# Optimization experiments

Measured on AMD Instinct MI355X. Metric: run time of the kernel, lower is better.

## Reference

```python
import jax, jax.numpy as jnp
import numpy as np
import math

GRID = 256       # grid_size
KMAX = 64        # max_elements_per_cell
RES = 512        # image resolution
SPAN = 4         # max grid cells per axis covered by one triangle bbox
NUM_VIEWS = 16
SCALE = 0.5


def _projection_matrix(x=0.5, n=1.5, f=100.0):
    return np.array([[n / x, 0.0, 0.0, 0.0],
                     [0.0, n / -x, 0.0, 0.0],
                     [0.0, 0.0, -(f + n) / (f - n), -(2.0 * f * n) / (f - n)],
                     [0.0, 0.0, -1.0, 0.0]], dtype=np.float32)


def _view_buffers(num_views, seed):
    rng = np.random.default_rng(seed)
    proj = _projection_matrix()
    mvps, lights = [], []
    for _ in range(num_views):
        u1, u2, u3 = rng.random(3)
        qx = math.sqrt(1.0 - u1) * math.sin(math.tau * u2)
        qy = math.sqrt(1.0 - u1) * math.cos(math.tau * u2)
        qz = math.sqrt(u1) * math.sin(math.tau * u3)
        qw = math.sqrt(u1) * math.cos(math.tau * u3)
        rot = np.array([[1 - 2 * (qy * qy + qz * qz), 2 * (qx * qy - qz * qw), 2 * (qx * qz + qy * qw)],
                        [2 * (qx * qy + qz * qw), 1 - 2 * (qx * qx + qz * qz), 2 * (qy * qz - qx * qw)],
                        [2 * (qx * qz - qy * qw), 2 * (qy * qz + qx * qw), 1 - 2 * (qx * qx + qy * qy)]], dtype=np.float32)
        rmat = np.eye(4, dtype=np.float32); rmat[:3, :3] = rot
        tmat = np.eye(4, dtype=np.float32); tmat[2, 3] = -4.0
        view = tmat @ rmat
        campos = np.linalg.inv(view)[:3, 3]
        light = -campos / (np.linalg.norm(campos) + 1e-8)
        mvps.append(proj @ view)
        lights.append(light.astype(np.float32))
    return np.stack(mvps).astype(np.float32), np.stack(lights).astype(np.float32)


def setup_inputs() -> dict:
    key = jax.random.key(0)
    k1, k2 = jax.random.split(key)
    F = 100_000
    # clustered per-triangle vertices -> small on-screen triangles (mesh-like locality)
    centers = jax.random.uniform(k1, (F, 1, 3), minval=-1.0, maxval=1.0)
    jitter = jax.random.normal(k2, (F, 3, 3)) * 0.02
    u = (centers + jitter).reshape(-1, 3).astype(jnp.float32)          # [3F,3]
    faces = jnp.arange(3 * F, dtype=jnp.int32).reshape(F, 3)
    mvps, light = _view_buffers(NUM_VIEWS, 42)
    return {"u": u,
            "mvps": jnp.asarray(mvps),
            "lightdir": jnp.asarray(light),
            "background_color": jnp.zeros(3, jnp.float32),
            "base_colors": jnp.ones((F, 3), jnp.float32),
            "faces": faces}


def _forward(u, mvps, lightdir, background_color, base_colors, faces):
    # _normalize_vertices
    v = u - u.mean(0, keepdims=True)
    span = jnp.maximum(v.max() - v.min(), 1e-6)
    v = v * (SCALE / span)
    Fn = faces.shape[0]
    # project with active view 0 (v_hom @ mvps[0].T, no perspective divide, as in source)
    v_hom = jnp.concatenate([v, jnp.ones((v.shape[0], 1), v.dtype)], axis=1)
    v_ndc = v_hom @ mvps[0].T                                          # [V,4]
    tris = v_ndc[faces]                                                # [F,3,4]
    wtri = v[faces]                                                    # [F,3,3]
    nrm = jnp.cross(wtri[:, 0] - wtri[:, 1], wtri[:, 2] - wtri[:, 1])
    nrm = nrm / (jnp.linalg.norm(nrm, axis=-1, keepdims=True) + 1e-10)
    z = tris[:, :, 2].mean(1)
    order = jnp.argsort(z)                                             # depth sort (near first)
    st = tris[order]
    sn = nrm[order]
    cp = (st[:, :, :2] + 1.0) * 0.5                                    # [F,3,2] control pts in [0,1]
    shading = jnp.clip(jnp.sum(-lightdir[0] * sn, axis=-1, keepdims=True), 0.0)
    colors = base_colors[order] * shading                              # [F,3]
    # --- grid acceleration structure build (scatter triangles into cells) ---
    lo = jnp.clip(jnp.floor(cp.min(1) * GRID).astype(jnp.int32), 0, GRID - 1)  # [F,2]
    hi = jnp.clip(jnp.floor(cp.max(1) * GRID).astype(jnp.int32), 0, GRID - 1)
    d = jnp.arange(SPAN, dtype=jnp.int32)
    cx = lo[:, 0:1] + d[None, :]                                       # [F,SPAN]
    cy = lo[:, 1:2] + d[None, :]
    valid = (cy[:, :, None] <= hi[:, 1:2, None]) & (cx[:, None, :] <= hi[:, 0:1].reshape(Fn, 1, 1) + 0 * cx[:, None, :])
    valid = (cy[:, :, None] <= hi[:, 1:2, None]) & (cx[:, None, :] <= hi[:, 0:1][:, :, None])
    cell = cy[:, :, None] * GRID + cx[:, None, :]                      # [F,SPAN,SPAN]
    NC = GRID * GRID
    cell = jnp.where(valid, cell, NC).reshape(-1)
    tri = jnp.broadcast_to(jnp.arange(Fn, dtype=jnp.int32)[:, None, None], (Fn, SPAN, SPAN)).reshape(-1)
    # sort (cell, depth-rank): tri ids are already depth-ordered
    keys = cell.astype(jnp.int64) * (Fn + 1) + tri
    ordk = jnp.argsort(keys)
    sc = cell[ordk]
    stri = tri[ordk]
    counts = jax.ops.segment_sum(jnp.ones_like(sc), sc, num_segments=NC + 1)
    starts = jnp.concatenate([jnp.zeros(1, counts.dtype), jnp.cumsum(counts)[:-1]])
    rank = jnp.arange(sc.shape[0], dtype=jnp.int32) - starts[sc].astype(jnp.int32)
    ok = (rank < KMAX) & (sc < NC)
    grid_elems = jnp.full((NC + 1, KMAX), -1, jnp.int32)
    grid_elems = grid_elems.at[jnp.where(ok, sc, NC), jnp.where(ok, rank, 0)].set(jnp.where(ok, stri, -1))
    # --- per-pixel rasterization via grid query ---
    px = (jnp.arange(RES, dtype=jnp.float32) + 0.5) / RES
    uu, vv = jnp.meshgrid(px, px, indexing='xy')
    P = jnp.stack([uu, vv], -1).reshape(-1, 2)                         # [P,2]
    ix = jnp.clip((P[:, 0] * GRID).astype(jnp.int32), 0, GRID - 1)
    iy = jnp.clip((P[:, 1] * GRID).astype(jnp.int32), 0, GRID - 1)
    elems = grid_elems[iy * GRID + ix]                                 # [P,K]
    e = jnp.maximum(elems, 0)
    tpts = cp[e]                                                       # [P,K,3,2]
    a, b, c = tpts[:, :, 0], tpts[:, :, 1], tpts[:, :, 2]
    pp = P[:, None, :]

    def cr(o, q, r):
        return (q[..., 0] - o[..., 0]) * (r[..., 1] - o[..., 1]) - (q[..., 1] - o[..., 1]) * (r[..., 0] - o[..., 0])

    e0 = cr(a, b, pp)
    e1 = cr(b, c, pp)
    e2 = cr(c, a, pp)
    inside = ((e0 >= 0) & (e1 >= 0) & (e2 >= 0)) | ((e0 <= 0) & (e1 <= 0) & (e2 <= 0))
    hit = inside & (elems >= 0)
    first = jnp.argmax(hit, axis=1)                                    # front-most (depth-sorted)
    anyhit = jnp.any(hit, axis=1)
    tid = e[jnp.arange(e.shape[0]), first]
    img = jnp.where(anyhit[:, None], colors[tid], background_color[None, :])
    return img.reshape(RES, RES, 3)


def reference(u, mvps, lightdir, background_color, base_colors, faces):
    return _forward(u, mvps, lightdir, background_color, base_colors, faces)
```

## Files before the change

kernel.cpp:

```cpp
#include <hip/hip_runtime.h>
#include <stdint.h>

#pragma clang fp contract(off)

#define GRIDN 256
#define NC (GRIDN * GRIDN)
#define RESN 512
#define RBLOCKS 256
#define CAP 1024
#define CPB 16
#define NB 64
#define NS 16
#define SBINS 2048

typedef unsigned short bfraw;
typedef unsigned short u16;

__device__ __forceinline__ float bf2f(bfraw h) {
    return __uint_as_float(((uint32_t)h) << 16);
}
__device__ __forceinline__ bfraw f2bf(float f) {
    uint32_t b = __float_as_uint(f);
    return (bfraw)((b + 0x7FFFu + ((b >> 16) & 1u)) >> 16);
}
__device__ __forceinline__ uint32_t fkey(float f) {
    uint32_t b = __float_as_uint(f);
    return (b & 0x80000000u) ? ~b : (b | 0x80000000u);
}

__global__ __launch_bounds__(256) void k_reduce1(const bfraw* __restrict__ u, int nrows,
                                                 double* __restrict__ psum,
                                                 float* __restrict__ pmin,
                                                 float* __restrict__ pmax) {
    __shared__ double ssum[256 * 3];
    __shared__ float smin[256 * 3];
    __shared__ float smax[256 * 3];
    int t = threadIdx.x;
    double s0 = 0.0, s1 = 0.0, s2 = 0.0;
    float mn0 = INFINITY, mn1 = INFINITY, mn2 = INFINITY;
    float mx0 = -INFINITY, mx1 = -INFINITY, mx2 = -INFINITY;
    for (int r = blockIdx.x * 256 + t; r < nrows; r += 256 * RBLOCKS) {
        float a = bf2f(u[3 * r + 0]);
        float b = bf2f(u[3 * r + 1]);
        float c = bf2f(u[3 * r + 2]);
        s0 += (double)a; s1 += (double)b; s2 += (double)c;
        mn0 = fminf(mn0, a); mx0 = fmaxf(mx0, a);
        mn1 = fminf(mn1, b); mx1 = fmaxf(mx1, b);
        mn2 = fminf(mn2, c); mx2 = fmaxf(mx2, c);
    }
    ssum[t * 3 + 0] = s0; ssum[t * 3 + 1] = s1; ssum[t * 3 + 2] = s2;
    smin[t * 3 + 0] = mn0; smin[t * 3 + 1] = mn1; smin[t * 3 + 2] = mn2;
    smax[t * 3 + 0] = mx0; smax[t * 3 + 1] = mx1; smax[t * 3 + 2] = mx2;
    __syncthreads();
    for (int st = 128; st > 0; st >>= 1) {
        if (t < st) {
            for (int c = 0; c < 3; c++) {
                ssum[t * 3 + c] += ssum[(t + st) * 3 + c];
                smin[t * 3 + c] = fminf(smin[t * 3 + c], smin[(t + st) * 3 + c]);
                smax[t * 3 + c] = fmaxf(smax[t * 3 + c], smax[(t + st) * 3 + c]);
            }
        }
        __syncthreads();
    }
    if (t == 0) {
        for (int c = 0; c < 3; c++) {
            psum[blockIdx.x * 3 + c] = ssum[c];
            pmin[blockIdx.x * 3 + c] = smin[c];
            pmax[blockIdx.x * 3 + c] = smax[c];
        }
    }
}

__global__ __launch_bounds__(256) void k_reduce2(const double* __restrict__ psum,
                                                 const float* __restrict__ pmin,
                                                 const float* __restrict__ pmax,
                                                 int nrows, float* __restrict__ cst) {
    __shared__ double ssum[256 * 3];
    __shared__ float smin[256 * 3];
    __shared__ float smax[256 * 3];
    int t = threadIdx.x;
    for (int c = 0; c < 3; c++) {
        ssum[t * 3 + c] = psum[t * 3 + c];
        smin[t * 3 + c] = pmin[t * 3 + c];
        smax[t * 3 + c] = pmax[t * 3 + c];
    }
    __syncthreads();
    for (int st = 128; st > 0; st >>= 1) {
        if (t < st) {
            for (int c = 0; c < 3; c++) {
                ssum[t * 3 + c] += ssum[(t + st) * 3 + c];
                smin[t * 3 + c] = fminf(smin[t * 3 + c], smin[(t + st) * 3 + c]);
                smax[t * 3 + c] = fmaxf(smax[t * 3 + c], smax[(t + st) * 3 + c]);
            }
        }
        __syncthreads();
    }
    if (t == 0) {
        float fn = (float)nrows;
        float m0 = (float)ssum[0] / fn;
        float m1 = (float)ssum[1] / fn;
        float m2 = (float)ssum[2] / fn;
        float vmax = fmaxf(fmaxf(smax[0] - m0, smax[1] - m1), smax[2] - m2);
        float vmin = fminf(fminf(smin[0] - m0, smin[1] - m1), smin[2] - m2);
        float span = fmaxf(vmax - vmin, 1e-06f);
        float s = 0.5f / span;
        cst[0] = m0; cst[1] = m1; cst[2] = m2; cst[3] = s;
    }
}

__global__ __launch_bounds__(256) void k_setup(const bfraw* __restrict__ u,
                                               const int* __restrict__ faces,
                                               const bfraw* __restrict__ mvp,
                                               const bfraw* __restrict__ light,
                                               const float* __restrict__ cst,
                                               int F,
                                               float* __restrict__ tcs,
                                               uint32_t* __restrict__ tz,
                                               uint32_t* __restrict__ tbox) {
    int f = blockIdx.x * 256 + threadIdx.x;
    if (f >= F) return;
    float m0 = cst[0], m1 = cst[1], m2 = cst[2], s = cst[3];
    float M[12];
    for (int i = 0; i < 12; i++) M[i] = bf2f(mvp[i]);

    float vx[3], vy[3], vz[3], cpx[3], cpy[3], zc[3];
    for (int j = 0; j < 3; j++) {
        int idx = faces[3 * f + j];
        float a = bf2f(u[3 * idx + 0]);
        float b = bf2f(u[3 * idx + 1]);
        float c = bf2f(u[3 * idx + 2]);
        float x = (a - m0) * s;
        float y = (b - m1) * s;
        float z = (c - m2) * s;
        vx[j] = x; vy[j] = y; vz[j] = z;
        float cx = fmaf(x, M[0], 0.0f);
        cx = fmaf(y, M[1], cx); cx = fmaf(z, M[2], cx); cx = cx + M[3];
        float cy = fmaf(x, M[4], 0.0f);
        cy = fmaf(y, M[5], cy); cy = fmaf(z, M[6], cy); cy = cy + M[7];
        float cz = fmaf(x, M[8], 0.0f);
        cz = fmaf(y, M[9], cz); cz = fmaf(z, M[10], cz); cz = cz + M[11];
        cpx[j] = (cx + 1.0f) * 0.5f;
        cpy[j] = (cy + 1.0f) * 0.5f;
        zc[j] = cz;
    }
    float zmean = ((zc[0] + zc[1]) + zc[2]) / 3.0f;

    float e1x = vx[0] - vx[1], e1y = vy[0] - vy[1], e1z = vz[0] - vz[1];
    float e2x = vx[2] - vx[1], e2y = vy[2] - vy[1], e2z = vz[2] - vz[1];
    float nx = e1y * e2z - e1z * e2y;
    float ny = e1z * e2x - e1x * e2z;
    float nz = e1x * e2y - e1y * e2x;
    float nn = nx * nx;
    nn = nn + ny * ny;
    nn = nn + nz * nz;
    float d = sqrtf(nn) + 1e-10f;
    float inx = nx / d, iny = ny / d, inz = nz / d;

    float l0 = bf2f(light[0]), l1 = bf2f(light[1]), l2 = bf2f(light[2]);
    float p0 = (-l0) * inx;
    float p1 = (-l1) * iny;
    float p2 = (-l2) * inz;
    float shading = fmaxf((p0 + p1) + p2, 0.0f);

    tcs[f * 8 + 0] = cpx[0]; tcs[f * 8 + 1] = cpy[0];
    tcs[f * 8 + 2] = cpx[1]; tcs[f * 8 + 3] = cpy[1];
    tcs[f * 8 + 4] = cpx[2]; tcs[f * 8 + 5] = cpy[2];
    tcs[f * 8 + 6] = shading;
    tcs[f * 8 + 7] = 0.0f;

    tz[f] = fkey(zmean);

    float mnx = fminf(fminf(cpx[0], cpx[1]), cpx[2]);
    float mny = fminf(fminf(cpy[0], cpy[1]), cpy[2]);
    float mxx = fmaxf(fmaxf(cpx[0], cpx[1]), cpx[2]);
    float mxy = fmaxf(fmaxf(cpy[0], cpy[1]), cpy[2]);
    int lox = (int)floorf(mnx * 256.0f); lox = lox < 0 ? 0 : (lox > 255 ? 255 : lox);
    int loy = (int)floorf(mny * 256.0f); loy = loy < 0 ? 0 : (loy > 255 ? 255 : loy);
    int hix = (int)floorf(mxx * 256.0f); hix = hix < 0 ? 0 : (hix > 255 ? 255 : hix);
    int hiy = (int)floorf(mxy * 256.0f); hiy = hiy < 0 ? 0 : (hiy > 255 ? 255 : hiy);
    int hx = hix < lox + 3 ? hix : lox + 3;
    int hy = hiy < loy + 3 ? hiy : loy + 3;
    tbox[f] = (uint32_t)lox | ((uint32_t)loy << 8) | ((uint32_t)hx << 16) | ((uint32_t)hy << 24);
}

__global__ __launch_bounds__(256) void k_count(const uint32_t* __restrict__ tbox,
                                               int F,
                                               u16* __restrict__ blockHist) {
    __shared__ uint32_t hist[SBINS];
    int b = blockIdx.x >> 4;
    int sl = blockIdx.x & (NS - 1);
    int chunk = (F + NB - 1) / NB;
    int fs = b * chunk;
    int fe = fs + chunk < F ? fs + chunk : F;
    int y0 = sl * 16, y1 = y0 + 15;
    for (int i = threadIdx.x; i < SBINS; i += 256) hist[i] = 0u;
    __syncthreads();
    for (int f = fs + threadIdx.x; f < fe; f += 256) {
        uint32_t bx = tbox[f];
        int lox = bx & 255, loy = (bx >> 8) & 255;
        int hx = (bx >> 16) & 255, hy = bx >> 24;
        int ys = loy > y0 ? loy : y0;
        int ye = hy < y1 ? hy : y1;
        for (int yy = ys; yy <= ye; yy++) {
            for (int xx = lox; xx <= hx; xx++) {
                uint32_t c = (uint32_t)(yy * GRIDN + xx) & 4095u;
                atomicAdd(&hist[c >> 1], 1u << (16u * (c & 1u)));
            }
        }
    }
    __syncthreads();
    uint32_t* dst = (uint32_t*)(blockHist + (size_t)b * NC) + sl * SBINS;
    for (int i = threadIdx.x; i < SBINS; i += 256) dst[i] = hist[i];
}

__global__ __launch_bounds__(1024) void k_scanA1(u16* __restrict__ blockHist,
                                                 uint32_t* __restrict__ cellOff,
                                                 uint32_t* __restrict__ blockSum) {
    __shared__ uint32_t sc[1024];
    int B = blockIdx.x, t = threadIdx.x;
    int c = B * 1024 + t;
    uint32_t tot = 0;
    for (int b = 0; b < NB; b++) {
        size_t o = (size_t)b * NC + c;
        uint32_t v = blockHist[o];
        blockHist[o] = (u16)tot;
        tot += v;
    }
    sc[t] = tot;
    __syncthreads();
    for (int st = 1; st < 1024; st <<= 1) {
        uint32_t a = 0;
        if (t >= st) a = sc[t - st];
        __syncthreads();
        if (t >= st) sc[t] += a;
        __syncthreads();
    }
    cellOff[c] = sc[t] - tot;
    if (t == 1023) blockSum[B] = sc[1023];
}

__global__ __launch_bounds__(1024) void k_scanB(uint32_t* __restrict__ cellOff,
                                                const uint32_t* __restrict__ blockSum) {
    __shared__ uint32_t pre[65];
    int B = blockIdx.x, t = threadIdx.x;
    if (t == 0) {
        uint32_t run = 0;
        for (int i = 0; i < 64; i++) { pre[i] = run; run += blockSum[i]; }
        pre[64] = run;
    }
    __syncthreads();
    cellOff[B * 1024 + t] += pre[B];
    if (B == 63 && t == 1023) cellOff[NC] = pre[64];
}

__global__ __launch_bounds__(256) void k_place(const uint32_t* __restrict__ tbox,
                                               const u16* __restrict__ blockHist,
                                               const uint32_t* __restrict__ cellOff,
                                               uint32_t* __restrict__ pairs,
                                               int F) {
    __shared__ uint32_t hist[SBINS];
    int b = blockIdx.x >> 4;
    int sl = blockIdx.x & (NS - 1);
    int chunk = (F + NB - 1) / NB;
    int fs = b * chunk;
    int fe = fs + chunk < F ? fs + chunk : F;
    int y0 = sl * 16, y1 = y0 + 15;
    uint32_t pcap = (uint32_t)F * 16u;
    for (int i = threadIdx.x; i < SBINS; i += 256) hist[i] = 0u;
    __syncthreads();
    for (int f = fs + threadIdx.x; f < fe; f += 256) {
        uint32_t bx = tbox[f];
        int lox = bx & 255, loy = (bx >> 8) & 255;
        int hx = (bx >> 16) & 255, hy = bx >> 24;
        int ys = loy > y0 ? loy : y0;
        int ye = hy < y1 ? hy : y1;
        for (int yy = ys; yy <= ye; yy++) {
            for (int xx = lox; xx <= hx; xx++) {
                uint32_t cell = (uint32_t)(yy * GRIDN + xx);
                uint32_t c = cell & 4095u;
                uint32_t sh = 16u * (c & 1u);
                uint32_t old = atomicAdd(&hist[c >> 1], 1u << sh);
                uint32_t r = (old >> sh) & 0xFFFFu;
                uint32_t pos = cellOff[cell] + (uint32_t)blockHist[(size_t)b * NC + cell] + r;
                if (pos < pcap) pairs[pos] = (uint32_t)f;
            }
        }
    }
}

__global__ __launch_bounds__(256) void k_cellsort(const uint32_t* __restrict__ cellOff,
                                                  const uint32_t* __restrict__ tz,
                                                  uint32_t* __restrict__ pairs,
                                                  int F) {
    __shared__ uint64_t lkeys[CAP];
    uint32_t pcap = (uint32_t)F * 16u;
    int t = threadIdx.x;
    int cell0 = blockIdx.x * CPB;
    for (int ci = 0; ci < CPB; ci++) {
        int cell = cell0 + ci;
        uint32_t off = cellOff[cell];
        uint32_t end = cellOff[cell + 1];
        if (off > pcap || end > pcap || end < off) continue;
        uint32_t n = end - off;
        if (n <= 64u) continue;
        uint32_t m = n > CAP ? CAP : n;
        for (uint32_t i = t; i < m; i += 256) {
            uint32_t id = pairs[off + i];
            if (id >= (uint32_t)F) id = 0;
            lkeys[i] = ((uint64_t)tz[id] << 32) | id;
        }
        __syncthreads();
        uint64_t k0 = ~0ull, k1 = ~0ull, k2 = ~0ull, k3 = ~0ull;
        uint32_t i0 = t, i1 = t + 256, i2 = t + 512, i3 = t + 768;
        if (i0 < m) k0 = lkeys[i0];
        if (i1 < m) k1 = lkeys[i1];
        if (i2 < m) k2 = lkeys[i2];
        if (i3 < m) k3 = lkeys[i3];
        uint32_t r0 = 0, r1 = 0, r2 = 0, r3 = 0;
        for (uint32_t j = 0; j < m; j++) {
            uint64_t kj = lkeys[j];
            r0 += (kj < k0) ? 1u : 0u;
            r1 += (kj < k1) ? 1u : 0u;
            r2 += (kj < k2) ? 1u : 0u;
            r3 += (kj < k3) ? 1u : 0u;
        }
        if (i0 < m && r0 < 64u) pairs[off + r0] = (uint32_t)(k0 & 0xFFFFFFFFu);
        if (i1 < m && r1 < 64u) pairs[off + r1] = (uint32_t)(k1 & 0xFFFFFFFFu);
        if (i2 < m && r2 < 64u) pairs[off + r2] = (uint32_t)(k2 & 0xFFFFFFFFu);
        if (i3 < m && r3 < 64u) pairs[off + r3] = (uint32_t)(k3 & 0xFFFFFFFFu);
        __syncthreads();
    }
}

__global__ __launch_bounds__(256) void k_raster(const float* __restrict__ tcs,
                                                const uint32_t* __restrict__ tz,
                                                const uint32_t* __restrict__ cellOff,
                                                const uint32_t* __restrict__ pairs,
                                                const bfraw* __restrict__ basec,
                                                const bfraw* __restrict__ bg,
                                                bfraw* __restrict__ out, int F) {
    int p = blockIdx.x * 256 + threadIdx.x;
    int col = p & (RESN - 1);
    int row = p >> 9;
    float px = ((float)col + 0.5f) / 512.0f;
    float py = ((float)row + 0.5f) / 512.0f;
    int cell = (row >> 1) * GRIDN + (col >> 1);
    uint32_t pcap = (uint32_t)F * 16u;
    uint32_t off = cellOff[cell];
    uint32_t end = cellOff[cell + 1];
    uint32_t m = 0;
    if (off <= pcap && end <= pcap && end >= off) {
        uint32_t n = end - off;
        m = n > 64u ? 64u : n;
    }
    uint64_t best = ~0ull;
    float bestSh = 0.0f;
    for (uint32_t k = 0; k < m; k++) {
        uint32_t id = pairs[off + k];
        if (id >= (uint32_t)F) continue;
        const float4 A = *(const float4*)(tcs + (size_t)id * 8);
        const float4 B = *(const float4*)(tcs + (size_t)id * 8 + 4);
        float ax = A.x, ay = A.y, bx = A.z, by = A.w, cx = B.x, cy = B.y;
        float e0 = (bx - ax) * (py - ay) - (by - ay) * (px - ax);
        float e1 = (cx - bx) * (py - by) - (cy - by) * (px - bx);
        float e2 = (ax - cx) * (py - cy) - (ay - cy) * (px - cx);
        bool inside = (e0 >= 0.0f && e1 >= 0.0f && e2 >= 0.0f) ||
                      (e0 <= 0.0f && e1 <= 0.0f && e2 <= 0.0f);
        if (inside) {
            uint64_t key = ((uint64_t)tz[id] << 32) | id;
            if (key < best) { best = key; bestSh = B.z; }
        }
    }
    float r, g, b;
    if (best != ~0ull) {
        uint32_t id = (uint32_t)(best & 0xFFFFFFFFu);
        r = bf2f(basec[3 * id + 0]) * bestSh;
        g = bf2f(basec[3 * id + 1]) * bestSh;
        b = bf2f(basec[3 * id + 2]) * bestSh;
    } else {
        r = bf2f(bg[0]); g = bf2f(bg[1]); b = bf2f(bg[2]);
    }
    int o = p * 3;
    out[o + 0] = f2bf(r);
    out[o + 1] = f2bf(g);
    out[o + 2] = f2bf(b);
}

__global__ __launch_bounds__(256) void k_diag(bfraw* __restrict__ out, float code) {
    out[blockIdx.x * 256 + threadIdx.x] = f2bf(code);
}

extern "C" void kernel_launch(void* const* d_in, const int* in_sizes, int n_in,
                              void* d_out, int out_size, void* d_ws, size_t ws_size,
                              hipStream_t stream) {
    const bfraw* u = (const bfraw*)d_in[0];
    const bfraw* mvps = (const bfraw*)d_in[1];
    const bfraw* light = (const bfraw*)d_in[2];
    const bfraw* bg = (const bfraw*)d_in[3];
    const bfraw* basec = (const bfraw*)d_in[4];
    const int* faces = (const int*)d_in[5];
    int nrows = in_sizes[0] / 3;
    int F = in_sizes[5] / 3;
    bfraw* out = (bfraw*)d_out;

    char* w = (char*)d_ws;
    size_t off = 0;
    auto alloc = [&](size_t bytes) -> void* {
        off = (off + 255) & ~(size_t)255;
        void* p = w + off;
        off += bytes;
        return p;
    };

    float* cst = (float*)alloc(4 * sizeof(float));
    double* psum = (double*)alloc((size_t)RBLOCKS * 3 * sizeof(double));
    float* pmin = (float*)alloc((size_t)RBLOCKS * 3 * sizeof(float));
    float* pmax = (float*)alloc((size_t)RBLOCKS * 3 * sizeof(float));
    float* tcs = (float*)alloc((size_t)F * 8 * sizeof(float));
    uint32_t* tz = (uint32_t*)alloc((size_t)F * sizeof(uint32_t));
    uint32_t* tbox = (uint32_t*)alloc((size_t)F * sizeof(uint32_t));
    u16* blockHist = (u16*)alloc((size_t)NB * NC * sizeof(u16));
    uint32_t* cellOff = (uint32_t*)alloc(((size_t)NC + 1) * sizeof(uint32_t));
    uint32_t* blockSum = (uint32_t*)alloc(64 * sizeof(uint32_t));
    uint32_t* pairs = (uint32_t*)alloc((size_t)F * 16 * sizeof(uint32_t));
    size_t needed = off;

    if (ws_size < needed) {
        float code = 20000.0f + (float)(ws_size >> 20);
        k_diag<<<(RESN * RESN * 3) / 256, 256, 0, stream>>>(out, code);
        return;
    }

    k_reduce1<<<RBLOCKS, 256, 0, stream>>>(u, nrows, psum, pmin, pmax);
    k_reduce2<<<1, 256, 0, stream>>>(psum, pmin, pmax, nrows, cst);
    k_setup<<<(F + 255) / 256, 256, 0, stream>>>(u, faces, mvps, light, cst, F,
                                                 tcs, tz, tbox);
    k_count<<<NB * NS, 256, 0, stream>>>(tbox, F, blockHist);
    k_scanA1<<<64, 1024, 0, stream>>>(blockHist, cellOff, blockSum);
    k_scanB<<<64, 1024, 0, stream>>>(cellOff, blockSum);
    k_place<<<NB * NS, 256, 0, stream>>>(tbox, blockHist, cellOff, pairs, F);
    k_cellsort<<<NC / CPB, 256, 0, stream>>>(cellOff, tz, pairs, F);
    k_raster<<<(RESN * RESN) / 256, 256, 0, stream>>>(tcs, tz, cellOff, pairs,
                                                      basec, bg, out, F);
}
```

Measured before the change: 154.6 us.

## Rasterize one grid cell per thread covering its four pixels; shrink binning blocks

The raster kernel now maps one thread to one grid cell. Each cell's triangle list is loaded once and tested against all four pixels in that cell, instead of four threads each reloading the same list. Edge deltas are computed once per triangle. NB also drops from 64 to 16, which changes the block count for the count and place kernels. The costs are fewer threads in the raster kernel (65536), uncoalesced strided output writes, and possible extra divergence.

Result: slower. 159.7 us (+3.3%).

```diff
diff --git a/kernel.cpp b/kernel.cpp
--- a/kernel.cpp
+++ b/kernel.cpp
@@ -9,7 +9,7 @@
 #define RBLOCKS 256
 #define CAP 1024
 #define CPB 16
-#define NB 64
+#define NB 16
 #define NS 16
 #define SBINS 2048
 
@@ -339,12 +339,12 @@
                                                 const bfraw* __restrict__ basec,
                                                 const bfraw* __restrict__ bg,
                                                 bfraw* __restrict__ out, int F) {
-    int p = blockIdx.x * 256 + threadIdx.x;
-    int col = p & (RESN - 1);
-    int row = p >> 9;
-    float px = ((float)col + 0.5f) / 512.0f;
-    float py = ((float)row + 0.5f) / 512.0f;
-    int cell = (row >> 1) * GRIDN + (col >> 1);
+    int cell = blockIdx.x * 256 + threadIdx.x;
+    int cy = cell >> 8, cx = cell & 255;
+    float px0 = ((float)(2 * cx) + 0.5f) / 512.0f;
+    float px1 = ((float)(2 * cx + 1) + 0.5f) / 512.0f;
+    float py0 = ((float)(2 * cy) + 0.5f) / 512.0f;
+    float py1 = ((float)(2 * cy + 1) + 0.5f) / 512.0f;
     uint32_t pcap = (uint32_t)F * 16u;
     uint32_t off = cellOff[cell];
     uint32_t end = cellOff[cell + 1];
@@ -353,37 +353,67 @@
         uint32_t n = end - off;
         m = n > 64u ? 64u : n;
     }
-    uint64_t best = ~0ull;
-    float bestSh = 0.0f;
+    uint64_t b00 = ~0ull, b01 = ~0ull, b10 = ~0ull, b11 = ~0ull;
+    float s00 = 0.0f, s01 = 0.0f, s10 = 0.0f, s11 = 0.0f;
     for (uint32_t k = 0; k < m; k++) {
         uint32_t id = pairs[off + k];
         if (id >= (uint32_t)F) continue;
         const float4 A = *(const float4*)(tcs + (size_t)id * 8);
         const float4 B = *(const float4*)(tcs + (size_t)id * 8 + 4);
-        float ax = A.x, ay = A.y, bx = A.z, by = A.w, cx = B.x, cy = B.y;
-        float e0 = (bx - ax) * (py - ay) - (by - ay) * (px - ax);
-        float e1 = (cx - bx) * (py - by) - (cy - by) * (px - bx);
-        float e2 = (ax - cx) * (py - cy) - (ay - cy) * (px - cx);
-        bool inside = (e0 >= 0.0f && e1 >= 0.0f && e2 >= 0.0f) ||
-                      (e0 <= 0.0f && e1 <= 0.0f && e2 <= 0.0f);
-        if (inside) {
+        float ax = A.x, ay = A.y, bx = A.z, by = A.w, tcx = B.x, tcy = B.y;
+        float dabx = bx - ax, daby = by - ay;
+        float dbcx = tcx - bx, dbcy = tcy - by;
+        float dcax = ax - tcx, dcay = ay - tcy;
+        float e0a, e1a, e2a;
+        bool in00, in01, in10, in11;
+        e0a = dabx * (py0 - ay) - daby * (px0 - ax);
+        e1a = dbcx * (py0 - by) - dbcy * (px0 - bx);
+        e2a = dcax * (py0 - tcy) - dcay * (px0 - tcx);
+        in00 = (e0a >= 0.0f && e1a >= 0.0f && e2a >= 0.0f) ||
+               (e0a <= 0.0f && e1a <= 0.0f && e2a <= 0.0f);
+        e0a = dabx * (py0 - ay) - daby * (px1 - ax);
+        e1a = dbcx * (py0 - by) - dbcy * (px1 - bx);
+        e2a = dcax * (py0 - tcy) - dcay * (px1 - tcx);
+        in01 = (e0a >= 0.0f && e1a >= 0.0f && e2a >= 0.0f) ||
+               (e0a <= 0.0f && e1a <= 0.0f && e2a <= 0.0f);
+        e0a = dabx * (py1 - ay) - daby * (px0 - ax);
+        e1a = dbcx * (py1 - by) - dbcy * (px0 - bx);
+        e2a = dcax * (py1 - tcy) - dcay * (px0 - tcx);
+        in10 = (e0a >= 0.0f && e1a >= 0.0f && e2a >= 0.0f) ||
+               (e0a <= 0.0f && e1a <= 0.0f && e2a <= 0.0f);
+        e0a = dabx * (py1 - ay) - daby * (px1 - ax);
+        e1a = dbcx * (py1 - by) - dbcy * (px1 - bx);
+        e2a = dcax * (py1 - tcy) - dcay * (px1 - tcx);
+        in11 = (e0a >= 0.0f && e1a >= 0.0f && e2a >= 0.0f) ||
+               (e0a <= 0.0f && e1a <= 0.0f && e2a <= 0.0f);
+        if (in00 | in01 | in10 | in11) {
             uint64_t key = ((uint64_t)tz[id] << 32) | id;
-            if (key < best) { best = key; bestSh = B.z; }
-        }
-    }
-    float r, g, b;
-    if (best != ~0ull) {
-        uint32_t id = (uint32_t)(best & 0xFFFFFFFFu);
-        r = bf2f(basec[3 * id + 0]) * bestSh;
-        g = bf2f(basec[3 * id + 1]) * bestSh;
-        b = bf2f(basec[3 * id + 2]) * bestSh;
-    } else {
-        r = bf2f(bg[0]); g = bf2f(bg[1]); b = bf2f(bg[2]);
-    }
-    int o = p * 3;
-    out[o + 0] = f2bf(r);
-    out[o + 1] = f2bf(g);
-    out[o + 2] = f2bf(b);
+            if (in00 && key < b00) { b00 = key; s00 = B.z; }
+            if (in01 && key < b01) { b01 = key; s01 = B.z; }
+            if (in10 && key < b10) { b10 = key; s10 = B.z; }
+            if (in11 && key < b11) { b11 = key; s11 = B.z; }
+        }
+    }
+    float bgr = bf2f(bg[0]), bgg = bf2f(bg[1]), bgb = bf2f(bg[2]);
+    uint64_t bests[4] = {b00, b01, b10, b11};
+    float shs[4] = {s00, s01, s10, s11};
+    for (int q = 0; q < 4; q++) {
+        int row = 2 * cy + (q >> 1);
+        int col = 2 * cx + (q & 1);
+        float r, g, b;
+        if (bests[q] != ~0ull) {
+            uint32_t id = (uint32_t)(bests[q] & 0xFFFFFFFFu);
+            r = bf2f(basec[3 * id + 0]) * shs[q];
+            g = bf2f(basec[3 * id + 1]) * shs[q];
+            b = bf2f(basec[3 * id + 2]) * shs[q];
+        } else {
+            r = bgr; g = bgg; b = bgb;
+        }
+        int o = (row * RESN + col) * 3;
+        out[o + 0] = f2bf(r);
+        out[o + 1] = f2bf(g);
+        out[o + 2] = f2bf(b);
+    }
 }
 
 __global__ __launch_bounds__(256) void k_diag(bfraw* __restrict__ out, float code) {
@@ -440,6 +470,5 @@
     k_scanB<<<64, 1024, 0, stream>>>(cellOff, blockSum);
     k_place<<<NB * NS, 256, 0, stream>>>(tbox, blockHist, cellOff, pairs, F);
     k_cellsort<<<NC / CPB, 256, 0, stream>>>(cellOff, tz, pairs, F);
-    k_raster<<<(RESN * RESN) / 256, 256, 0, stream>>>(tcs, tz, cellOff, pairs,
-                                                      basec, bg, out, F);
-}
+    k_raster<<<NC / 256, 256, 0, stream>>>(tcs, tz, cellOff, pairs, basec, bg, out, F);
+}
```
